# Kernel tuning notes

Hardware: AMD Instinct MI355X
Metric: run time of the kernel (lower is better)

The kernel has to match this reference:

```python
import jax, jax.numpy as jnp
import numpy as np

T_TEMP = 1.0
MIN_VAR = 1e-06
EPS = 1e-10
HIDDEN = 64
OBS_C = 4


def setup_inputs() -> dict:
    key = jax.random.key(0)
    k1, k2, k3, k4 = jax.random.split(key, 4)
    B, S = 128, 2048
    return {
        "observations": jax.random.normal(k1, (B, S, OBS_C), dtype=jnp.float32),
        "base_transition_logits": jax.random.normal(k2, (HIDDEN, HIDDEN), dtype=jnp.float32),
        "initial_logits": jax.random.normal(k3, (HIDDEN,), dtype=jnp.float32),
        "emission_means": jax.random.normal(k4, (HIDDEN, OBS_C), dtype=jnp.float32),
        "emission_log_vars": jnp.zeros((HIDDEN, OBS_C), dtype=jnp.float32),
    }


def _emission_log_probs(obs, means, log_vars):
    # obs: [B,S,C], means/log_vars: [H,C]
    # log N(obs | mu_h, var_h) summed over channels C, without materializing [B,S,H,C]:
    # -0.5 * sum_c [ log(2*pi*v_hc) + (x_bsc - mu_hc)^2 / v_hc ]
    var = jnp.exp(log_vars) + MIN_VAR            # [H,C]
    inv_var = 1.0 / var
    log_norm = jnp.log(2.0 * jnp.pi * var).sum(-1)                     # [H]
    quad = (
        jnp.einsum("bsc,hc->bsh", obs * obs, inv_var)
        - 2.0 * jnp.einsum("bsc,hc->bsh", obs, means * inv_var)
        + (means * means * inv_var).sum(-1)                            # [H]
    )
    return -0.5 * (log_norm + quad)              # [B,S,H]


def reference(observations, base_transition_logits, initial_logits,
              emission_means, emission_log_vars):
    B, S, _ = observations.shape
    em = _emission_log_probs(observations[:, :, :OBS_C], emission_means, emission_log_vars)  # [B,S,H]

    trans = jax.nn.softmax(base_transition_logits / T_TEMP, axis=-1)   # [H,H]
    trans_log = jnp.log(trans + EPS)                                   # [H,H]
    init_dist = jax.nn.softmax(initial_logits / T_TEMP, axis=-1)

    alpha0 = jnp.log(init_dist + EPS)[None, :] + em[:, 0, :]           # [B,H]

    def step(a_prev, em_t):
        # logsumexp over source state i: a_prev[b,i] + trans_log[i,j]
        a = jax.nn.logsumexp(a_prev[:, :, None] + trans_log[None, :, :], axis=1) + em_t
        return a, a

    em_rest = jnp.swapaxes(em[:, 1:, :], 0, 1)                         # [S-1,B,H]
    _, alphas = jax.lax.scan(step, alpha0, em_rest)                    # [S-1,B,H]
    alpha = jnp.concatenate([alpha0[None], alphas], axis=0)            # [S,B,H]
    alpha = jnp.swapaxes(alpha, 0, 1)                                  # [B,S,H]
    log_likelihood = jax.nn.logsumexp(alpha[:, -1, :], axis=-1)        # [B]
    return alpha, log_likelihood
```

## Files before the change

kernel.cpp:

```cpp
#include <hip/hip_runtime.h>
#include <math.h>

#define BB 128
#define SS 2048
#define HH 64
#define CC 4
#define EPSQ 1e-10f
#define NT ((size_t)BB * SS * HH)

typedef float f2 __attribute__((ext_vector_type(2)));
typedef float f4 __attribute__((ext_vector_type(4)));


__global__ __launch_bounds__(64) void hmm_setup(const float* __restrict__ base,
                                                const float* __restrict__ init,
                                                float* __restrict__ Qt,
                                                float* __restrict__ D) {
    const int i = threadIdx.x;
    float mx = -INFINITY;
    for (int k = 0; k < HH; ++k) mx = fmaxf(mx, base[i * HH + k]);
    float z = 0.f;
    for (int k = 0; k < HH; ++k) z += expf(base[i * HH + k] - mx);
    float invz = 1.f / z;
    for (int k = 0; k < HH; ++k) Qt[k * HH + i] = expf(base[i * HH + k] - mx) * invz + EPSQ;
    float x = init[i];
    float m2 = x;
    for (int d = 1; d < 64; d <<= 1) m2 = fmaxf(m2, __shfl_xor(m2, d, 64));
    float e = expf(x - m2);
    float zz = e;
    for (int d = 1; d < 64; d <<= 1) zz += __shfl_xor(zz, d, 64);
    D[i] = e / zz + EPSQ;
}

__device__ __forceinline__ float emv(const f4 x, const f4 a, const f4 q, float c0) {
    float em = c0;
    em = fmaf(fmaf(q.x, x.x, a.x), x.x, em);
    em = fmaf(fmaf(q.y, x.y, a.y), x.y, em);
    em = fmaf(fmaf(q.z, x.z, a.z), x.z, em);
    em = fmaf(fmaf(q.w, x.w, a.w), x.w, em);
    return em;
}

#define PK_MUL(d, a, b) asm("v_pk_mul_f32 %0, %1, %2" : "=v"(d) : "v"(a), "v"(b))
#define PK_FMA(d, a, b) asm("v_pk_fma_f32 %0, %1, %2, %0" : "+v"(d) : "v"(a), "v"(b))
#define PK_ADD(d, a, b) asm("v_pk_add_f32 %0, %1, %2" : "=v"(d) : "v"(a), "v"(b))

template <int P>
__device__ __forceinline__ void hmm_step(int t, int j, float& u, float& gE, float& gcur,
                                         float& A, const f2 (&qr)[32],
                                         float (&Ubuf)[2][HH], const f4* OBS,
                                         const f4 ea, const f4 eq, float ec,
                                         float* __restrict__ alpha_b) {
    Ubuf[P][j] = u;
    A -= __logf(gcur);

    const f4* Up = (const f4*)Ubuf[P];
    f2 acc0, acc1, acc2, acc3;
    {
        f4 v = Up[0];
        f2 lo = __builtin_shufflevector(v, v, 0, 1);
        f2 hi = __builtin_shufflevector(v, v, 2, 3);
        PK_MUL(acc0, qr[0], lo);
        PK_MUL(acc1, qr[1], hi);
    }
    {
        f4 v = Up[1];
        f2 lo = __builtin_shufflevector(v, v, 0, 1);
        f2 hi = __builtin_shufflevector(v, v, 2, 3);
        PK_MUL(acc2, qr[2], lo);
        PK_MUL(acc3, qr[3], hi);
    }
#pragma unroll
    for (int k = 2; k < 16; ++k) {
        f4 v = Up[k];
        f2 lo = __builtin_shufflevector(v, v, 0, 1);
        f2 hi = __builtin_shufflevector(v, v, 2, 3);
        if (k & 1) {
            PK_FMA(acc2, qr[2 * k], lo);
            PK_FMA(acc3, qr[2 * k + 1], hi);
        } else {
            PK_FMA(acc0, qr[2 * k], lo);
            PK_FMA(acc1, qr[2 * k + 1], hi);
        }
    }
    const int tn = (t < SS - 1) ? t + 1 : SS - 1;
    const f4 xn = OBS[tn];

    f2 sa, sb, s2;
    PK_ADD(sa, acc0, acc1);
    PK_ADD(sb, acc2, acc3);
    PK_ADD(s2, sa, sb);
    const float s = s2.x + s2.y;
    const float un = s * gE;

    alpha_b[(size_t)t * HH + j] = A + __logf(un);

    gcur = __builtin_amdgcn_rcpf(__int_as_float(
        __builtin_amdgcn_readfirstlane(__float_as_int(un))));
    gE = gcur * __expf(emv(xn, ea, eq, ec));
    u = un;
}

__global__ __launch_bounds__(64, 1) void hmm_scan(const float* __restrict__ obs,
                                                  const float* __restrict__ means,
                                                  const float* __restrict__ logvars,
                                                  const float* __restrict__ Qt,
                                                  const float* __restrict__ D,
                                                  float* __restrict__ out) {
    const int b = blockIdx.x;
    const int j = threadIdx.x;
    __shared__ f4 OBS[SS];
    __shared__ float Ubuf[2][HH];

    const f4* obs4 = (const f4*)obs + (size_t)b * SS;
#pragma unroll 8
    for (int t = j; t < SS; t += 64) OBS[t] = obs4[t];

    f2 qr[32];
    const f4* qrow = (const f4*)(Qt + (size_t)j * HH);
#pragma unroll
    for (int k = 0; k < 16; ++k) {
        f4 v = qrow[k];
        qr[2 * k]     = __builtin_shufflevector(v, v, 0, 1);
        qr[2 * k + 1] = __builtin_shufflevector(v, v, 2, 3);
    }

    const f4 mu = ((const f4*)means)[j];
    const f4 lv = ((const f4*)logvars)[j];
    f4 ea, eq;
    float ec = 0.f;
    {
        float v0 = __expf(lv.x) + 1e-6f, v1 = __expf(lv.y) + 1e-6f;
        float v2 = __expf(lv.z) + 1e-6f, v3 = __expf(lv.w) + 1e-6f;
        float i0 = 1.f / v0, i1 = 1.f / v1, i2 = 1.f / v2, i3 = 1.f / v3;
        ea.x = mu.x * i0; ea.y = mu.y * i1; ea.z = mu.z * i2; ea.w = mu.w * i3;
        eq.x = -0.5f * i0; eq.y = -0.5f * i1; eq.z = -0.5f * i2; eq.w = -0.5f * i3;
        ec += logf(6.2831853071795864f * v0) + mu.x * mu.x * i0;
        ec += logf(6.2831853071795864f * v1) + mu.y * mu.y * i1;
        ec += logf(6.2831853071795864f * v2) + mu.z * mu.z * i2;
        ec += logf(6.2831853071795864f * v3) + mu.w * mu.w * i3;
        ec = -0.5f * ec;
    }

    float* alpha_b = out + (size_t)b * SS * HH;

    float u = D[j] * __expf(emv(OBS[0], ea, eq, ec));
    alpha_b[j] = __logf(u);
    float A = 0.f;
    float gcur = __builtin_amdgcn_rcpf(__int_as_float(
        __builtin_amdgcn_readfirstlane(__float_as_int(u))));
    float gE = gcur * __expf(emv(OBS[1], ea, eq, ec));

#pragma unroll 4
    for (int t = 1; t + 1 < SS; t += 2) {
        hmm_step<1>(t, j, u, gE, gcur, A, qr, Ubuf, OBS, ea, eq, ec, alpha_b);
        hmm_step<0>(t + 1, j, u, gE, gcur, A, qr, Ubuf, OBS, ea, eq, ec, alpha_b);
    }
    hmm_step<1>(SS - 1, j, u, gE, gcur, A, qr, Ubuf, OBS, ea, eq, ec, alpha_b);

    float ssum = u;
    for (int d = 1; d < 64; d <<= 1) ssum += __shfl_xor(ssum, d, 64);
    if (j == 0) out[NT + b] = A + __logf(ssum);
}

extern "C" void kernel_launch(void* const* d_in, const int* in_sizes, int n_in,
                              void* d_out, int out_size, void* d_ws, size_t ws_size,
                              hipStream_t stream) {
    (void)in_sizes; (void)n_in; (void)out_size; (void)ws_size;
    const float* obs     = (const float*)d_in[0];
    const float* base    = (const float*)d_in[1];
    const float* init    = (const float*)d_in[2];
    const float* means   = (const float*)d_in[3];
    const float* logvars = (const float*)d_in[4];
    float* out = (float*)d_out;

    float* Qt = (float*)d_ws;
    float* D  = (float*)((char*)d_ws + 16384);

    hmm_setup<<<1, 64, 0, stream>>>(base, init, Qt, D);
    hmm_scan<<<BB, 64, 0, stream>>>(obs, means, logvars, Qt, D, out);
}
```

Baseline: 525.4 us.

## Split matvec across lane quads with DPP reduction and LDS emission staging

Restructures the per-step 64x64 matrix-vector product so each group of four lanes computes four output states over a 16-element slice of the source vector, then combines the partial sums with DPP cross-lane adds. Each lane now reads 16 LDS values per step instead of 64, and the transition matrix is stored in natural row order. Emission likelihoods for the next step are staged through LDS. This shortens the serial dependency chain per time step, at the cost of extra DPP ops, lane-select logic and an LDS round trip for emissions, with no explicit barrier visible between the LDS writes and reads.

```diff
diff --git a/kernel.cpp b/kernel.cpp
--- a/kernel.cpp
+++ b/kernel.cpp
@@ -4,7 +4,6 @@
 #define BB 128
 #define SS 2048
 #define HH 64
-#define CC 4
 #define EPSQ 1e-10f
 #define NT ((size_t)BB * SS * HH)
 
@@ -14,7 +13,7 @@
 
 __global__ __launch_bounds__(64) void hmm_setup(const float* __restrict__ base,
                                                 const float* __restrict__ init,
-                                                float* __restrict__ Qt,
+                                                float* __restrict__ Qn,
                                                 float* __restrict__ D) {
     const int i = threadIdx.x;
     float mx = -INFINITY;
@@ -22,7 +21,7 @@
     float z = 0.f;
     for (int k = 0; k < HH; ++k) z += expf(base[i * HH + k] - mx);
     float invz = 1.f / z;
-    for (int k = 0; k < HH; ++k) Qt[k * HH + i] = expf(base[i * HH + k] - mx) * invz + EPSQ;
+    for (int k = 0; k < HH; ++k) Qn[i * HH + k] = expf(base[i * HH + k] - mx) * invz + EPSQ;
     float x = init[i];
     float m2 = x;
     for (int d = 1; d < 64; d <<= 1) m2 = fmaxf(m2, __shfl_xor(m2, d, 64));
@@ -43,90 +42,53 @@
 
 #define PK_MUL(d, a, b) asm("v_pk_mul_f32 %0, %1, %2" : "=v"(d) : "v"(a), "v"(b))
 #define PK_FMA(d, a, b) asm("v_pk_fma_f32 %0, %1, %2, %0" : "+v"(d) : "v"(a), "v"(b))
-#define PK_ADD(d, a, b) asm("v_pk_add_f32 %0, %1, %2" : "=v"(d) : "v"(a), "v"(b))
 
-template <int P>
-__device__ __forceinline__ void hmm_step(int t, int j, float& u, float& gE, float& gcur,
-                                         float& A, const f2 (&qr)[32],
-                                         float (&Ubuf)[2][HH], const f4* OBS,
-                                         const f4 ea, const f4 eq, float ec,
-                                         float* __restrict__ alpha_b) {
-    Ubuf[P][j] = u;
-    A -= __logf(gcur);
+#define DPPADD(v, CTRL)                                                              \
+    {                                                                                \
+        int _a = __builtin_amdgcn_mov_dpp(__float_as_int(v.x), CTRL, 0xF, 0xF, true); \
+        int _b = __builtin_amdgcn_mov_dpp(__float_as_int(v.y), CTRL, 0xF, 0xF, true); \
+        v.x += __int_as_float(_a);                                                   \
+        v.y += __int_as_float(_b);                                                   \
+    }
 
-    const f4* Up = (const f4*)Ubuf[P];
-    f2 acc0, acc1, acc2, acc3;
-    {
-        f4 v = Up[0];
-        f2 lo = __builtin_shufflevector(v, v, 0, 1);
-        f2 hi = __builtin_shufflevector(v, v, 2, 3);
-        PK_MUL(acc0, qr[0], lo);
-        PK_MUL(acc1, qr[1], hi);
-    }
-    {
-        f4 v = Up[1];
-        f2 lo = __builtin_shufflevector(v, v, 0, 1);
-        f2 hi = __builtin_shufflevector(v, v, 2, 3);
-        PK_MUL(acc2, qr[2], lo);
-        PK_MUL(acc3, qr[3], hi);
-    }
-#pragma unroll
-    for (int k = 2; k < 16; ++k) {
-        f4 v = Up[k];
-        f2 lo = __builtin_shufflevector(v, v, 0, 1);
-        f2 hi = __builtin_shufflevector(v, v, 2, 3);
-        if (k & 1) {
-            PK_FMA(acc2, qr[2 * k], lo);
-            PK_FMA(acc3, qr[2 * k + 1], hi);
-        } else {
-            PK_FMA(acc0, qr[2 * k], lo);
-            PK_FMA(acc1, qr[2 * k + 1], hi);
-        }
-    }
-    const int tn = (t < SS - 1) ? t + 1 : SS - 1;
-    const f4 xn = OBS[tn];
-
-    f2 sa, sb, s2;
-    PK_ADD(sa, acc0, acc1);
-    PK_ADD(sb, acc2, acc3);
-    PK_ADD(s2, sa, sb);
-    const float s = s2.x + s2.y;
-    const float un = s * gE;
-
-    alpha_b[(size_t)t * HH + j] = A + __logf(un);
-
-    gcur = __builtin_amdgcn_rcpf(__int_as_float(
-        __builtin_amdgcn_readfirstlane(__float_as_int(un))));
-    gE = gcur * __expf(emv(xn, ea, eq, ec));
-    u = un;
-}
+#define LO2(v) __builtin_shufflevector(v, v, 0, 1)
+#define HI2(v) __builtin_shufflevector(v, v, 2, 3)
 
 __global__ __launch_bounds__(64, 1) void hmm_scan(const float* __restrict__ obs,
                                                   const float* __restrict__ means,
                                                   const float* __restrict__ logvars,
-                                                  const float* __restrict__ Qt,
+                                                  const float* __restrict__ Qn,
                                                   const float* __restrict__ D,
                                                   float* __restrict__ out) {
     const int b = blockIdx.x;
-    const int j = threadIdx.x;
+    const int l = threadIdx.x;
+    const int g = l >> 2;
+    const int s = l & 3;
+    const bool b0 = (l & 1) != 0;
+    const bool b1 = (l & 2) != 0;
+
     __shared__ f4 OBS[SS];
-    __shared__ float Ubuf[2][HH];
+    __shared__ float U_lds[HH];
+    __shared__ float E_lds[HH];
 
     const f4* obs4 = (const f4*)obs + (size_t)b * SS;
 #pragma unroll 8
-    for (int t = j; t < SS; t += 64) OBS[t] = obs4[t];
+    for (int t = l; t < SS; t += 64) OBS[t] = obs4[t];
 
-    f2 qr[32];
-    const f4* qrow = (const f4*)(Qt + (size_t)j * HH);
+    f2 q0[8], q1[8], q2[8], q3[8];
+    const float* qbase = Qn + (size_t)(16 * s) * HH + 4 * g;
 #pragma unroll
-    for (int k = 0; k < 16; ++k) {
-        f4 v = qrow[k];
-        qr[2 * k]     = __builtin_shufflevector(v, v, 0, 1);
-        qr[2 * k + 1] = __builtin_shufflevector(v, v, 2, 3);
+    for (int m = 0; m < 8; ++m) {
+        f4 rA = *(const f4*)(qbase + (size_t)(2 * m) * HH);
+        f4 rB = *(const f4*)(qbase + (size_t)(2 * m + 1) * HH);
+        q0[m] = (f2){rA.x, rB.x};
+        q1[m] = (f2){rA.y, rB.y};
+        q2[m] = (f2){rA.z, rB.z};
+        q3[m] = (f2){rA.w, rB.w};
     }
 
-    const f4 mu = ((const f4*)means)[j];
-    const f4 lv = ((const f4*)logvars)[j];
+    const f4 mu = ((const f4*)means)[l];
+    const f4 lv = ((const f4*)logvars)[l];
     f4 ea, eq;
     float ec = 0.f;
     {
@@ -144,23 +106,74 @@
 
     float* alpha_b = out + (size_t)b * SS * HH;
 
-    float u = D[j] * __expf(emv(OBS[0], ea, eq, ec));
-    alpha_b[j] = __logf(u);
+    float u0 = D[l] * __expf(emv(OBS[0], ea, eq, ec));
+    U_lds[l] = u0;
+    alpha_b[l] = __logf(u0);
+    E_lds[l] = __expf(emv(OBS[1], ea, eq, ec));
     float A = 0.f;
     float gcur = __builtin_amdgcn_rcpf(__int_as_float(
-        __builtin_amdgcn_readfirstlane(__float_as_int(u))));
-    float gE = gcur * __expf(emv(OBS[1], ea, eq, ec));
+        __builtin_amdgcn_readfirstlane(__float_as_int(u0))));
 
-#pragma unroll 4
-    for (int t = 1; t + 1 < SS; t += 2) {
-        hmm_step<1>(t, j, u, gE, gcur, A, qr, Ubuf, OBS, ea, eq, ec, alpha_b);
-        hmm_step<0>(t + 1, j, u, gE, gcur, A, qr, Ubuf, OBS, ea, eq, ec, alpha_b);
+    f4 un;
+#pragma unroll 2
+    for (int t = 1; t < SS; ++t) {
+        const f4* Uq = (const f4*)U_lds + 4 * s;
+        f4 U0 = Uq[0], U1 = Uq[1], U2 = Uq[2], U3 = Uq[3];
+        f4 e4 = *(const f4*)(E_lds + 4 * g);
+
+        A -= __logf(gcur);
+        const float gE0 = gcur * e4.x, gE1 = gcur * e4.y;
+        const float gE2 = gcur * e4.z, gE3 = gcur * e4.w;
+
+        f2 uu0 = LO2(U0), uu1 = HI2(U0), uu2 = LO2(U1), uu3 = HI2(U1);
+        f2 uu4 = LO2(U2), uu5 = HI2(U2), uu6 = LO2(U3), uu7 = HI2(U3);
+        f2 acc0, acc1, acc2, acc3;
+        PK_MUL(acc0, q0[0], uu0); PK_MUL(acc1, q1[0], uu0);
+        PK_MUL(acc2, q2[0], uu0); PK_MUL(acc3, q3[0], uu0);
+        PK_FMA(acc0, q0[1], uu1); PK_FMA(acc1, q1[1], uu1);
+        PK_FMA(acc2, q2[1], uu1); PK_FMA(acc3, q3[1], uu1);
+        PK_FMA(acc0, q0[2], uu2); PK_FMA(acc1, q1[2], uu2);
+        PK_FMA(acc2, q2[2], uu2); PK_FMA(acc3, q3[2], uu2);
+        PK_FMA(acc0, q0[3], uu3); PK_FMA(acc1, q1[3], uu3);
+        PK_FMA(acc2, q2[3], uu3); PK_FMA(acc3, q3[3], uu3);
+        PK_FMA(acc0, q0[4], uu4); PK_FMA(acc1, q1[4], uu4);
+        PK_FMA(acc2, q2[4], uu4); PK_FMA(acc3, q3[4], uu4);
+        PK_FMA(acc0, q0[5], uu5); PK_FMA(acc1, q1[5], uu5);
+        PK_FMA(acc2, q2[5], uu5); PK_FMA(acc3, q3[5], uu5);
+        PK_FMA(acc0, q0[6], uu6); PK_FMA(acc1, q1[6], uu6);
+        PK_FMA(acc2, q2[6], uu6); PK_FMA(acc3, q3[6], uu6);
+        PK_FMA(acc0, q0[7], uu7); PK_FMA(acc1, q1[7], uu7);
+        PK_FMA(acc2, q2[7], uu7); PK_FMA(acc3, q3[7], uu7);
+
+        f2 sA = (f2){acc0.x + acc0.y, acc1.x + acc1.y};
+        f2 sB = (f2){acc2.x + acc2.y, acc3.x + acc3.y};
+        DPPADD(sA, 0xB1); DPPADD(sB, 0xB1);
+        DPPADD(sA, 0x4E); DPPADD(sB, 0x4E);
+
+        un.x = sA.x * gE0;
+        un.y = sA.y * gE1;
+        un.z = sB.x * gE2;
+        un.w = sB.y * gE3;
+
+        if ((l & 3) == 0) *(f4*)(U_lds + 4 * g) = un;
+
+        const float usel = b1 ? (b0 ? un.w : un.z) : (b0 ? un.y : un.x);
+        alpha_b[(size_t)t * HH + l] = A + __logf(usel);
+
+        gcur = __builtin_amdgcn_rcpf(__int_as_float(
+            __builtin_amdgcn_readfirstlane(__float_as_int(un.x))));
+
+        const int tn = (t < SS - 1) ? t + 1 : SS - 1;
+        const f4 xn = OBS[tn];
+        E_lds[l] = __expf(emv(xn, ea, eq, ec));
     }
-    hmm_step<1>(SS - 1, j, u, gE, gcur, A, qr, Ubuf, OBS, ea, eq, ec, alpha_b);
 
-    float ssum = u;
-    for (int d = 1; d < 64; d <<= 1) ssum += __shfl_xor(ssum, d, 64);
-    if (j == 0) out[NT + b] = A + __logf(ssum);
+    float tot = (un.x + un.y) + (un.z + un.w);
+    tot += __shfl_xor(tot, 4, 64);
+    tot += __shfl_xor(tot, 8, 64);
+    tot += __shfl_xor(tot, 16, 64);
+    tot += __shfl_xor(tot, 32, 64);
+    if (l == 0) out[NT + b] = A + __logf(tot);
 }
 
 extern "C" void kernel_launch(void* const* d_in, const int* in_sizes, int n_in,
@@ -174,9 +187,9 @@
     const float* logvars = (const float*)d_in[4];
     float* out = (float*)d_out;
 
-    float* Qt = (float*)d_ws;
+    float* Qn = (float*)d_ws;
     float* D  = (float*)((char*)d_ws + 16384);
 
-    hmm_setup<<<1, 64, 0, stream>>>(base, init, Qt, D);
-    hmm_scan<<<BB, 64, 0, stream>>>(obs, means, logvars, Qt, D, out);
+    hmm_setup<<<1, 64, 0, stream>>>(base, init, Qn, D);
+    hmm_scan<<<BB, 64, 0, stream>>>(obs, means, logvars, Qn, D, out);
 }
```

Measured after the change: 658.4 us. +25.3%, slower.

## Split each transition dot product across lane pairs with DPP reduction

Applied to the files above, without the earlier changes.

Each pair of lanes now works on two destination states. Each lane reads only half of the shared scaled-alpha vector and computes partial dot products for both rows, then combines the halves with a DPP cross-lane add. This halves the LDS reads per lane per step and shrinks the register-held transition rows, cutting the latency of the serial recurrence. The double-buffered LDS slot becomes a single buffer, and the running log-offset now comes from lane 0's log value, which changes the final log-likelihood bookkeeping.

```diff
diff --git a/kernel.cpp b/kernel.cpp
--- a/kernel.cpp
+++ b/kernel.cpp
@@ -4,7 +4,6 @@
 #define BB 128
 #define SS 2048
 #define HH 64
-#define CC 4
 #define EPSQ 1e-10f
 #define NT ((size_t)BB * SS * HH)
 
@@ -45,61 +44,16 @@
 #define PK_FMA(d, a, b) asm("v_pk_fma_f32 %0, %1, %2, %0" : "+v"(d) : "v"(a), "v"(b))
 #define PK_ADD(d, a, b) asm("v_pk_add_f32 %0, %1, %2" : "=v"(d) : "v"(a), "v"(b))
 
-template <int P>
-__device__ __forceinline__ void hmm_step(int t, int j, float& u, float& gE, float& gcur,
-                                         float& A, const f2 (&qr)[32],
-                                         float (&Ubuf)[2][HH], const f4* OBS,
-                                         const f4 ea, const f4 eq, float ec,
-                                         float* __restrict__ alpha_b) {
-    Ubuf[P][j] = u;
-    A -= __logf(gcur);
+#define DPP_X1_ADD(s)                                                                  \
+    {                                                                                  \
+        int _v = __builtin_amdgcn_mov_dpp(__float_as_int(s), 0xB1, 0xF, 0xF, true);    \
+        s += __int_as_float(_v);                                                       \
+    }
 
-    const f4* Up = (const f4*)Ubuf[P];
-    f2 acc0, acc1, acc2, acc3;
-    {
-        f4 v = Up[0];
-        f2 lo = __builtin_shufflevector(v, v, 0, 1);
-        f2 hi = __builtin_shufflevector(v, v, 2, 3);
-        PK_MUL(acc0, qr[0], lo);
-        PK_MUL(acc1, qr[1], hi);
-    }
-    {
-        f4 v = Up[1];
-        f2 lo = __builtin_shufflevector(v, v, 0, 1);
-        f2 hi = __builtin_shufflevector(v, v, 2, 3);
-        PK_MUL(acc2, qr[2], lo);
-        PK_MUL(acc3, qr[3], hi);
-    }
-#pragma unroll
-    for (int k = 2; k < 16; ++k) {
-        f4 v = Up[k];
-        f2 lo = __builtin_shufflevector(v, v, 0, 1);
-        f2 hi = __builtin_shufflevector(v, v, 2, 3);
-        if (k & 1) {
-            PK_FMA(acc2, qr[2 * k], lo);
-            PK_FMA(acc3, qr[2 * k + 1], hi);
-        } else {
-            PK_FMA(acc0, qr[2 * k], lo);
-            PK_FMA(acc1, qr[2 * k + 1], hi);
-        }
-    }
-    const int tn = (t < SS - 1) ? t + 1 : SS - 1;
-    const f4 xn = OBS[tn];
+#define LO2(v) __builtin_shufflevector(v, v, 0, 1)
+#define HI2(v) __builtin_shufflevector(v, v, 2, 3)
 
-    f2 sa, sb, s2;
-    PK_ADD(sa, acc0, acc1);
-    PK_ADD(sb, acc2, acc3);
-    PK_ADD(s2, sa, sb);
-    const float s = s2.x + s2.y;
-    const float un = s * gE;
-
-    alpha_b[(size_t)t * HH + j] = A + __logf(un);
-
-    gcur = __builtin_amdgcn_rcpf(__int_as_float(
-        __builtin_amdgcn_readfirstlane(__float_as_int(un))));
-    gE = gcur * __expf(emv(xn, ea, eq, ec));
-    u = un;
-}
+#define RFL(x) __int_as_float(__builtin_amdgcn_readfirstlane(__float_as_int(x)))
 
 __global__ __launch_bounds__(64, 1) void hmm_scan(const float* __restrict__ obs,
                                                   const float* __restrict__ means,
@@ -108,25 +62,27 @@
                                                   const float* __restrict__ D,
                                                   float* __restrict__ out) {
     const int b = blockIdx.x;
-    const int j = threadIdx.x;
+    const int l = threadIdx.x;
+    const int p = l & 1;
+    const int e = l & ~1;
+
     __shared__ f4 OBS[SS];
-    __shared__ float Ubuf[2][HH];
+    __shared__ float U_lds[HH];
 
     const f4* obs4 = (const f4*)obs + (size_t)b * SS;
 #pragma unroll 8
-    for (int t = j; t < SS; t += 64) OBS[t] = obs4[t];
+    for (int t = l; t < SS; t += 64) OBS[t] = obs4[t];
 
-    f2 qr[32];
-    const f4* qrow = (const f4*)(Qt + (size_t)j * HH);
+    f4 QA[8], QB[8];
+    {
+        const f4* qa = (const f4*)(Qt + (size_t)e * HH + 32 * p);
+        const f4* qb = (const f4*)(Qt + (size_t)(e + 1) * HH + 32 * p);
 #pragma unroll
-    for (int k = 0; k < 16; ++k) {
-        f4 v = qrow[k];
-        qr[2 * k]     = __builtin_shufflevector(v, v, 0, 1);
-        qr[2 * k + 1] = __builtin_shufflevector(v, v, 2, 3);
+        for (int k = 0; k < 8; ++k) { QA[k] = qa[k]; QB[k] = qb[k]; }
     }
 
-    const f4 mu = ((const f4*)means)[j];
-    const f4 lv = ((const f4*)logvars)[j];
+    const f4 mu = ((const f4*)means)[l];
+    const f4 lv = ((const f4*)logvars)[l];
     f4 ea, eq;
     float ec = 0.f;
     {
@@ -144,23 +100,64 @@
 
     float* alpha_b = out + (size_t)b * SS * HH;
 
-    float u = D[j] * __expf(emv(OBS[0], ea, eq, ec));
-    alpha_b[j] = __logf(u);
-    float A = 0.f;
-    float gcur = __builtin_amdgcn_rcpf(__int_as_float(
-        __builtin_amdgcn_readfirstlane(__float_as_int(u))));
+    float u = D[l] * __expf(emv(OBS[0], ea, eq, ec));
+    U_lds[l] = u;
+    float lg = __logf(u);
+    alpha_b[l] = lg;
+    float A = RFL(lg);
+    float gcur = __builtin_amdgcn_rcpf(RFL(u));
     float gE = gcur * __expf(emv(OBS[1], ea, eq, ec));
 
-#pragma unroll 4
-    for (int t = 1; t + 1 < SS; t += 2) {
-        hmm_step<1>(t, j, u, gE, gcur, A, qr, Ubuf, OBS, ea, eq, ec, alpha_b);
-        hmm_step<0>(t + 1, j, u, gE, gcur, A, qr, Ubuf, OBS, ea, eq, ec, alpha_b);
+#pragma unroll 2
+    for (int t = 1; t < SS; ++t) {
+        const f4* Uq = (const f4*)U_lds + 8 * p;
+        f4 U0 = Uq[0], U1 = Uq[1], U2 = Uq[2], U3 = Uq[3];
+        f4 U4 = Uq[4], U5 = Uq[5], U6 = Uq[6], U7 = Uq[7];
+
+        f2 aA0, aA1, aB0, aB1;
+        PK_MUL(aA0, LO2(QA[0]), LO2(U0)); PK_MUL(aA1, HI2(QA[0]), HI2(U0));
+        PK_MUL(aB0, LO2(QB[0]), LO2(U0)); PK_MUL(aB1, HI2(QB[0]), HI2(U0));
+        PK_FMA(aA0, LO2(QA[1]), LO2(U1)); PK_FMA(aA1, HI2(QA[1]), HI2(U1));
+        PK_FMA(aB0, LO2(QB[1]), LO2(U1)); PK_FMA(aB1, HI2(QB[1]), HI2(U1));
+        PK_FMA(aA0, LO2(QA[2]), LO2(U2)); PK_FMA(aA1, HI2(QA[2]), HI2(U2));
+        PK_FMA(aB0, LO2(QB[2]), LO2(U2)); PK_FMA(aB1, HI2(QB[2]), HI2(U2));
+        PK_FMA(aA0, LO2(QA[3]), LO2(U3)); PK_FMA(aA1, HI2(QA[3]), HI2(U3));
+        PK_FMA(aB0, LO2(QB[3]), LO2(U3)); PK_FMA(aB1, HI2(QB[3]), HI2(U3));
+        PK_FMA(aA0, LO2(QA[4]), LO2(U4)); PK_FMA(aA1, HI2(QA[4]), HI2(U4));
+        PK_FMA(aB0, LO2(QB[4]), LO2(U4)); PK_FMA(aB1, HI2(QB[4]), HI2(U4));
+        PK_FMA(aA0, LO2(QA[5]), LO2(U5)); PK_FMA(aA1, HI2(QA[5]), HI2(U5));
+        PK_FMA(aB0, LO2(QB[5]), LO2(U5)); PK_FMA(aB1, HI2(QB[5]), HI2(U5));
+        PK_FMA(aA0, LO2(QA[6]), LO2(U6)); PK_FMA(aA1, HI2(QA[6]), HI2(U6));
+        PK_FMA(aB0, LO2(QB[6]), LO2(U6)); PK_FMA(aB1, HI2(QB[6]), HI2(U6));
+        PK_FMA(aA0, LO2(QA[7]), LO2(U7)); PK_FMA(aA1, HI2(QA[7]), HI2(U7));
+        PK_FMA(aB0, LO2(QB[7]), LO2(U7)); PK_FMA(aB1, HI2(QB[7]), HI2(U7));
+
+        f2 sA, sB;
+        PK_ADD(sA, aA0, aA1);
+        PK_ADD(sB, aB0, aB1);
+        float s_e = sA.x + sA.y;
+        float s_o = sB.x + sB.y;
+        DPP_X1_ADD(s_e);
+        DPP_X1_ADD(s_o);
+        const float sd = p ? s_o : s_e;
+        const float un = sd * gE;
+        U_lds[l] = un;
+
+        lg = __logf(un);
+        const float av = A + lg;
+        alpha_b[(size_t)t * HH + l] = av;
+        A = RFL(av);
+        gcur = __builtin_amdgcn_rcpf(RFL(un));
+        const int tn = (t < SS - 1) ? t + 1 : SS - 1;
+        const f4 xn = OBS[tn];
+        gE = gcur * __expf(emv(xn, ea, eq, ec));
+        u = un;
     }
-    hmm_step<1>(SS - 1, j, u, gE, gcur, A, qr, Ubuf, OBS, ea, eq, ec, alpha_b);
 
     float ssum = u;
     for (int d = 1; d < 64; d <<= 1) ssum += __shfl_xor(ssum, d, 64);
-    if (j == 0) out[NT + b] = A + __logf(ssum);
+    const float lg0 = RFL(lg);
+    if (l == 0) out[NT + b] = (A - lg0) + __logf(ssum);
 }
 
 extern "C" void kernel_launch(void* const* d_in, const int* in_sizes, int n_in,
```

After: 471.9 us. -10.2%, faster.
